# Kernel tuning notes

Measured on AMD Instinct MI355X. Metric: run time of the kernel, lower is better.

The kernel has to match this reference:

```python
import math
import jax, jax.numpy as jnp
import numpy as np

EPS = 1e-08
W_BLK = 256  # covers max window w = exp(log 255) + 1 = 256


def _l2norm(x):
    n = jnp.linalg.norm(x, axis=-1, keepdims=True)
    return x / jnp.maximum(n, EPS)


def setup_inputs() -> dict:
    key = jax.random.key(0)
    ks = jax.random.split(key, 7)
    B, T, Dm, H = 2, 4096, 1024, 16
    scale = 1.0 / math.sqrt(Dm)
    return {
        "query": jax.random.normal(ks[0], (B, T, Dm), jnp.float32),
        "key": jax.random.normal(ks[1], (B, T, Dm), jnp.float32),
        "value": jax.random.normal(ks[2], (B, T, Dm), jnp.float32),
        "Wq": jax.random.normal(ks[3], (Dm, Dm), jnp.float32) * scale,
        "Wk": jax.random.normal(ks[4], (Dm, Dm), jnp.float32) * scale,
        "Wv": jax.random.normal(ks[5], (Dm, Dm), jnp.float32) * scale,
        "Wo": jax.random.normal(ks[6], (Dm, Dm), jnp.float32) * scale,
        "s_v": jnp.linspace(0.0, math.log(255.0), H).astype(jnp.float32),
        "s_r": jnp.zeros((H,), jnp.float32),
    }


def _screening_forward(query, key, value, Wq, Wk, Wv, Wo, s_v, s_r):
    B, T, Dm = query.shape
    H = s_v.shape[0]
    D = Dm // H

    def proj(x, Wm):  # nn.Linear (no bias): x @ W^T, then split heads -> [B,H,T,D]
        return (x @ Wm.T).reshape(B, T, H, D).transpose(0, 2, 1, 3)

    q = _l2norm(proj(query, Wq))
    k = _l2norm(proj(key, Wk))
    v = _l2norm(proj(value, Wv))

    w = jnp.exp(s_v) + 1.0  # [H] window widths, <= 256
    r = jnp.exp(s_r) + 1.0  # [H] screening sharpness

    Wb = W_BLK
    nb = T // Wb
    qb = q.reshape(B, H, nb, Wb, D)
    kb = k.reshape(B, H, nb, Wb, D)
    vb = v.reshape(B, H, nb, Wb, D)
    # each query block attends to its own block + previous block (window <= Wb)
    kprev = jnp.pad(kb, ((0, 0), (0, 0), (1, 0), (0, 0), (0, 0)))[:, :, :nb]
    vprev = jnp.pad(vb, ((0, 0), (0, 0), (1, 0), (0, 0), (0, 0)))[:, :, :nb]
    kc = jnp.concatenate([kprev, kb], axis=3)  # [B,H,nb,2W,D]
    vc = jnp.concatenate([vprev, vb], axis=3)

    sim = jnp.einsum('bhnid,bhnjd->bhnij', qb, kc)  # [B,H,nb,W,2W]

    ii = jnp.arange(Wb)[:, None]
    jj = jnp.arange(2 * Wb)[None, :]
    rel = (jj - (Wb + ii)).astype(jnp.float32)  # [W,2W] relative offset j-i
    wb_ = w[:, None, None]  # [H,1,1]
    cos_m = 0.5 * (jnp.cos(jnp.pi * rel[None] / wb_) + 1.0)  # [H,W,2W]
    in_w = (rel[None] > -wb_) & (rel[None] <= 0.0)  # causal window
    softmask = cos_m * in_w.astype(sim.dtype)  # [H,W,2W]
    # block 0 has no previous block: first Wb key slots invalid there
    blk_valid = ((jnp.arange(nb)[:, None] > 0) | (jnp.arange(2 * Wb)[None, :] >= Wb))

    alpha = jax.nn.relu(1.0 - r[None, :, None, None, None] * (1.0 - sim)) ** 2
    alpha = alpha * softmask[None, :, None] * blk_valid.astype(sim.dtype)[None, None, :, None, :]

    out = jnp.einsum('bhnij,bhnjd->bhnid', alpha, vc).reshape(B, H, T, D)
    # TanhNorm: smoothly bound vector magnitude (tanh of the L2 norm)
    n = jnp.linalg.norm(out, axis=-1, keepdims=True)
    out = out * jnp.tanh(n) / (n + EPS)
    out = out.transpose(0, 2, 1, 3).reshape(B, T, Dm)
    return out @ Wo.T


def reference(query, key, value, Wq, Wk, Wv, Wo, s_v, s_r):
    return _screening_forward(query, key, value, Wq, Wk, Wv, Wo, s_v, s_r)
```

## Files before the change

### kernel.cpp

```cpp
#include <hip/hip_runtime.h>
#include <math.h>

#ifndef M_PI
#define M_PI 3.14159265358979323846
#endif

typedef short bf16x8 __attribute__((ext_vector_type(8)));
typedef _Float16 f16x8 __attribute__((ext_vector_type(8)));
typedef float f32x4 __attribute__((ext_vector_type(4)));

#define LDS_STRIDE 40

union FragU { uint4 u; bf16x8 f; };
union F16U { uint4 u; f16x8 f; _Float16 h[8]; };

__device__ __forceinline__ unsigned rn_hi(float x) {
    unsigned u = __float_as_uint(x);
    unsigned r = u + 0x7FFFu + ((u >> 16) & 1u);
    return r & 0xFFFF0000u;
}

__global__ void mask_tab_kernel(const float* __restrict__ s_v, float* __restrict__ tab) {
    int h = blockIdx.x;
    int idx = threadIdx.x;
    float w = expf(s_v[h]) + 1.0f;
    float rel = (float)(idx - 255);
    float val = 0.0f;
    if (rel > -w) {
        val = 0.5f * (cosf((float)M_PI * rel / w) + 1.0f);
    }
    tab[h * 256 + idx] = val;
}

__device__ __forceinline__ void split8_f16(_Float16* ph, _Float16* pl, int off,
                                           f32x4 x0, f32x4 x1) {
    float xs[8] = {x0[0], x0[1], x0[2], x0[3], x1[0], x1[1], x1[2], x1[3]};
    F16U H, L;
#pragma unroll
    for (int e = 0; e < 8; e++) {
        _Float16 h = (_Float16)xs[e];
        _Float16 l = (_Float16)(xs[e] - (float)h);
        H.h[e] = h;
        L.h[e] = l;
    }
    *(uint4*)(ph + off) = H.u;
    *(uint4*)(pl + off) = L.u;
}

__device__ __forceinline__ void load_ab(const float* aptr, const float* bptr, int kt,
                                        f32x4* ab, f32x4* bb) {
#pragma unroll
    for (int m = 0; m < 4; m++) {
        ab[m] = *(const f32x4*)(aptr + kt + m * 4);
        bb[m] = *(const f32x4*)(bptr + kt + m * 4);
    }
}

__device__ __forceinline__ void stage_ab(_Float16* AhP, _Float16* AlP,
                                         _Float16* BhP, _Float16* BlP, int soff,
                                         const f32x4* ab, const f32x4* bb) {
    split8_f16(AhP, AlP, soff,     ab[0], ab[1]);
    split8_f16(AhP, AlP, soff + 8, ab[2], ab[3]);
    split8_f16(BhP, BlP, soff,     bb[0], bb[1]);
    split8_f16(BhP, BlP, soff + 8, bb[2], bb[3]);
}

__device__ __forceinline__ void compute_tile(const _Float16* AhP, const _Float16* AlP,
                                             const _Float16* BhP, const _Float16* BlP,
                                             int aoff, int boff, f32x4 acc[4][4]) {
#define MFMA_TILE(AF, BF)                                                            \
    do {                                                                             \
        _Pragma("unroll") for (int fr = 0; fr < 4; fr++)                             \
            _Pragma("unroll") for (int fc = 0; fc < 4; fc++)                         \
                acc[fr][fc] = __builtin_amdgcn_mfma_f32_16x16x32_f16(                \
                    AF[fr], BF[fc], acc[fr][fc], 0, 0, 0);                           \
    } while (0)
    f16x8 ah[4], bh[4], t1[4], t2[4];
#pragma unroll
    for (int f = 0; f < 4; f++) {
        ah[f] = *(const f16x8*)&AhP[aoff + f * 16 * LDS_STRIDE];
        bh[f] = *(const f16x8*)&BhP[boff + f * 16 * LDS_STRIDE];
    }
    MFMA_TILE(ah, bh);
#pragma unroll
    for (int f = 0; f < 4; f++)
        t1[f] = *(const f16x8*)&BlP[boff + f * 16 * LDS_STRIDE];
    MFMA_TILE(ah, t1);
#pragma unroll
    for (int f = 0; f < 4; f++)
        t2[f] = *(const f16x8*)&AlP[aoff + f * 16 * LDS_STRIDE];
    MFMA_TILE(t2, bh);
#undef MFMA_TILE
}

template <int PERM>
__global__ __launch_bounds__(256, 2) void gemm_f16x3(const float* __restrict__ A,
                                                     const float* __restrict__ Bm,
                                                     float* __restrict__ C,
                                                     int M, int N, int K) {
    __shared__ _Float16 Ah[2][128 * LDS_STRIDE];
    __shared__ _Float16 Al[2][128 * LDS_STRIDE];
    __shared__ _Float16 Bh[2][128 * LDS_STRIDE];
    __shared__ _Float16 Bl[2][128 * LDS_STRIDE];

    const int tid = threadIdx.x;
    const int bid = blockIdx.x;
    const int swz = (bid & 7) * ((int)gridDim.x >> 3) + (bid >> 3);
    const int brow = (swz >> 3) * 128;
    const int bcol = (swz & 7) * 128;

    const int lane = tid & 63;
    const int wv = tid >> 6;
    const int wr = wv >> 1;
    const int wc = wv & 1;

    const int srow = tid >> 1;
    const int skb = (tid & 1) * 16;
    const float* aptr = A + (size_t)(brow + srow) * K + skb;
    const float* bptr = Bm + (size_t)(bcol + srow) * K + skb;
    const int soff = srow * LDS_STRIDE + skb;

    const int l15 = lane & 15;
    const int k8 = (lane >> 4) * 8;
    const int aoff = (wr * 64 + l15) * LDS_STRIDE + k8;
    const int boff = (wc * 64 + l15) * LDS_STRIDE + k8;

    f32x4 acc[4][4];
#pragma unroll
    for (int a = 0; a < 4; a++)
#pragma unroll
        for (int b = 0; b < 4; b++) acc[a][b] = (f32x4)(0.0f);

    const int nt = K >> 5;
    f32x4 a0[4], b0[4], a1[4], b1[4];
    load_ab(aptr, bptr, 0, a0, b0);
    load_ab(aptr, bptr, 32, a1, b1);
    stage_ab(Ah[0], Al[0], Bh[0], Bl[0], soff, a0, b0);
    __syncthreads();

#pragma unroll 1
    for (int t = 0; t < nt; t += 2) {
        if (t + 2 < nt) load_ab(aptr, bptr, (t + 2) * 32, a0, b0);
        stage_ab(Ah[1], Al[1], Bh[1], Bl[1], soff, a1, b1);
        compute_tile(Ah[0], Al[0], Bh[0], Bl[0], aoff, boff, acc);
        __syncthreads();
        if (t + 3 < nt) load_ab(aptr, bptr, (t + 3) * 32, a1, b1);
        if (t + 2 < nt) stage_ab(Ah[0], Al[0], Bh[0], Bl[0], soff, a0, b0);
        compute_tile(Ah[1], Al[1], Bh[1], Bl[1], aoff, boff, acc);
        __syncthreads();
    }

    if (PERM == 1) {
#pragma unroll
        for (int fr = 0; fr < 4; fr++) {
#pragma unroll
            for (int r = 0; r < 4; r++) {
                float p = 0.0f;
#pragma unroll
                for (int fc = 0; fc < 4; fc++)
                    p = fmaf(acc[fr][fc][r], acc[fr][fc][r], p);
                p += __shfl_xor(p, 1);
                p += __shfl_xor(p, 2);
                p += __shfl_xor(p, 4);
                p += __shfl_xor(p, 8);
                float inv = 1.0f / fmaxf(sqrtf(p), 1e-8f);
#pragma unroll
                for (int fc = 0; fc < 4; fc++) acc[fr][fc][r] *= inv;
            }
        }
    }

    const int rsub = (lane >> 4) * 4;
#pragma unroll
    for (int fr = 0; fr < 4; fr++) {
#pragma unroll
        for (int fc = 0; fc < 4; fc++) {
            f32x4 v = acc[fr][fc];
            const int i0 = brow + wr * 64 + fr * 16 + rsub;
            const int j = bcol + wc * 64 + fc * 16 + l15;
            if (PERM == 0) {
#pragma unroll
                for (int r = 0; r < 4; r++) C[(size_t)(i0 + r) * N + j] = v[r];
            } else {
                const int h = j >> 6;
                const int d = j & 63;
#pragma unroll
                for (int r = 0; r < 4; r++) {
                    const int i = i0 + r;
                    const int b = i >> 12;
                    const int t = i & 4095;
                    C[(((size_t)(b * 16 + h) * 4096 + t) * 64 + d)] = v[r];
                }
            }
        }
    }
}

__global__ __launch_bounds__(256, 3) void attn_kernel(
        const float* __restrict__ q, const float* __restrict__ k,
        const float* __restrict__ v, const float* __restrict__ s_v,
        const float* __restrict__ s_r, const float* __restrict__ mask_tab,
        float* __restrict__ out) {
    __shared__ unsigned short Kh[32 * 72];
    __shared__ unsigned short Kl[32 * 72];
    __shared__ unsigned short Vh[64 * 40];
    __shared__ unsigned short Vl[64 * 40];
    __shared__ unsigned int   aB[4][32 * 33];
    __shared__ float          msk[256];

    const int bx = blockIdx.x;
    const int h   = bx & 15;
    const int n   = (bx >> 4) & 15;
    const int sub = (bx >> 8) & 1;
    const int b   = bx >> 9;
    const int bh = b * 16 + h;
    const int tid = threadIdx.x;
    const int lane = tid & 63;
    const int wid = tid >> 6;
    const int l15 = lane & 15;
    const int g = lane >> 4;

    msk[tid] = mask_tab[h * 256 + tid];
    const float w = expf(s_v[h]) + 1.0f;
    const float rh = expf(s_r[h]) + 1.0f;

    const int row0 = n * 256 + sub * 128;
    const float* qbase = q + (size_t)bh * 4096 * 64;
    const float* kbase = k + (size_t)bh * 4096 * 64;
    const float* vbase = v + (size_t)bh * 4096 * 64;

    bf16x8 qh[2][2], ql[2][2];
#pragma unroll
    for (int f = 0; f < 2; f++) {
#pragma unroll
        for (int ks = 0; ks < 2; ks++) {
            const float* src = qbase + (size_t)(row0 + wid * 32 + f * 16 + l15) * 64
                               + ks * 32 + g * 8;
            f32x4 x0 = *(const f32x4*)src;
            f32x4 x1 = *(const f32x4*)(src + 4);
            float xs[8] = {x0[0], x0[1], x0[2], x0[3], x1[0], x1[1], x1[2], x1[3]};
            unsigned hb[8], lb[8];
#pragma unroll
            for (int e = 0; e < 8; e++) {
                hb[e] = rn_hi(xs[e]);
                lb[e] = rn_hi(xs[e] - __uint_as_float(hb[e]));
            }
            FragU th, tl;
            th.u = make_uint4((hb[0] >> 16) | hb[1], (hb[2] >> 16) | hb[3],
                              (hb[4] >> 16) | hb[5], (hb[6] >> 16) | hb[7]);
            tl.u = make_uint4((lb[0] >> 16) | lb[1], (lb[2] >> 16) | lb[3],
                              (lb[4] >> 16) | lb[5], (lb[6] >> 16) | lb[7]);
            qh[f][ks] = th.f;
            ql[f][ks] = tl.f;
        }
    }

    int jlo = (int)floorf(256.0f + (float)(sub * 128) - w) + 1;
    if (jlo < 0) jlo = 0;
    if (n == 0 && jlo < 256) jlo = 256;
    jlo &= ~31;
    const int jhi = 256 + sub * 128 + 127;

    const int iw0 = sub * 128 + wid * 32;

    f32x4 acc[2][4];
#pragma unroll
    for (int a = 0; a < 2; a++)
#pragma unroll
        for (int d = 0; d < 4; d++) acc[a][d] = (f32x4)(0.0f);

    const int kj = tid >> 3;
    const int kd = (tid & 7) * 8;
    const int vj = tid & 31;
    const int vd = (tid >> 5) * 8;

    f32x4 kr0, kr1, vr0, vr1;
    {
        const float* ks = kbase + (size_t)((n - 1) * 256 + jlo + kj) * 64 + kd;
        const float* vs = vbase + (size_t)((n - 1) * 256 + jlo + vj) * 64 + vd;
        kr0 = *(const f32x4*)ks;  kr1 = *(const f32x4*)(ks + 4);
        vr0 = *(const f32x4*)vs;  vr1 = *(const f32x4*)(vs + 4);
    }

    for (int jt = jlo; jt <= jhi; jt += 32) {
        __syncthreads();
        {
            float xs[8] = {kr0[0], kr0[1], kr0[2], kr0[3], kr1[0], kr1[1], kr1[2], kr1[3]};
            unsigned hb[8], lb[8];
#pragma unroll
            for (int e = 0; e < 8; e++) {
                hb[e] = rn_hi(xs[e]);
                lb[e] = rn_hi(xs[e] - __uint_as_float(hb[e]));
            }
            *(uint4*)&Kh[kj * 72 + kd] =
                make_uint4((hb[0] >> 16) | hb[1], (hb[2] >> 16) | hb[3],
                           (hb[4] >> 16) | hb[5], (hb[6] >> 16) | hb[7]);
            *(uint4*)&Kl[kj * 72 + kd] =
                make_uint4((lb[0] >> 16) | lb[1], (lb[2] >> 16) | lb[3],
                           (lb[4] >> 16) | lb[5], (lb[6] >> 16) | lb[7]);
        }
        {
            float xs[8] = {vr0[0], vr0[1], vr0[2], vr0[3], vr1[0], vr1[1], vr1[2], vr1[3]};
#pragma unroll
            for (int e = 0; e < 8; e++) {
                unsigned hbv = rn_hi(xs[e]);
                unsigned lbv = rn_hi(xs[e] - __uint_as_float(hbv));
                Vh[(vd + e) * 40 + vj] = (unsigned short)(hbv >> 16);
                Vl[(vd + e) * 40 + vj] = (unsigned short)(lbv >> 16);
            }
        }
        if (jt + 32 <= jhi) {
            const float* ks = kbase + (size_t)((n - 1) * 256 + jt + 32 + kj) * 64 + kd;
            const float* vs = vbase + (size_t)((n - 1) * 256 + jt + 32 + vj) * 64 + vd;
            kr0 = *(const f32x4*)ks;  kr1 = *(const f32x4*)(ks + 4);
            vr0 = *(const f32x4*)vs;  vr1 = *(const f32x4*)(vs + 4);
        }
        __syncthreads();

        const bool live = ((float)(jt + 31) > 256.0f + (float)iw0 - w) &&
                          (jt <= 256 + iw0 + 31);
        if (live) {
            f32x4 sim[2][2];
#pragma unroll
            for (int jf = 0; jf < 2; jf++)
#pragma unroll
                for (int f = 0; f < 2; f++) sim[jf][f] = (f32x4)(0.0f);

#pragma unroll
            for (int jf = 0; jf < 2; jf++) {
#pragma unroll
                for (int ks = 0; ks < 2; ks++) {
                    bf16x8 kah = *(const bf16x8*)&Kh[(jf * 16 + l15) * 72 + ks * 32 + g * 8];
                    bf16x8 kal = *(const bf16x8*)&Kl[(jf * 16 + l15) * 72 + ks * 32 + g * 8];
#pragma unroll
                    for (int f = 0; f < 2; f++) {
                        sim[jf][f] = __builtin_amdgcn_mfma_f32_16x16x32_bf16(
                            kah, qh[f][ks], sim[jf][f], 0, 0, 0);
                        sim[jf][f] = __builtin_amdgcn_mfma_f32_16x16x32_bf16(
                            kah, ql[f][ks], sim[jf][f], 0, 0, 0);
                        sim[jf][f] = __builtin_amdgcn_mfma_f32_16x16x32_bf16(
                            kal, qh[f][ks], sim[jf][f], 0, 0, 0);
                    }
                }
            }

#pragma unroll
            for (int jf = 0; jf < 2; jf++) {
#pragma unroll
                for (int f = 0; f < 2; f++) {
#pragma unroll
                    for (int r = 0; r < 4; r++) {
                        const int jloc = jf * 16 + g * 4 + r;
                        const int iloc = f * 16 + l15;
                        const int relv = (jt + jloc) - 256 - (sub * 128 + wid * 32 + iloc);
                        float m = (relv >= -255 && relv <= 0) ? msk[relv + 255] : 0.0f;
                        float t1 = 1.0f - rh * (1.0f - sim[jf][f][r]);
                        t1 = fmaxf(t1, 0.0f);
                        float alpha = t1 * t1 * m;
                        unsigned ahb = rn_hi(alpha);
                        unsigned alb = rn_hi(alpha - __uint_as_float(ahb));
                        aB[wid][jloc * 33 + iloc] = ahb | (alb >> 16);
                    }
                }
            }

#pragma unroll
            for (int f = 0; f < 2; f++) {
                unsigned a8[8];
#pragma unroll
                for (int e = 0; e < 8; e++)
                    a8[e] = aB[wid][(g * 8 + e) * 33 + f * 16 + l15];
                FragU th, tl;
                th.u = make_uint4((a8[0] >> 16) | (a8[1] & 0xFFFF0000u),
                                  (a8[2] >> 16) | (a8[3] & 0xFFFF0000u),
                                  (a8[4] >> 16) | (a8[5] & 0xFFFF0000u),
                                  (a8[6] >> 16) | (a8[7] & 0xFFFF0000u));
                tl.u = make_uint4((a8[0] << 16 >> 16) | (a8[1] << 16),
                                  (a8[2] << 16 >> 16) | (a8[3] << 16),
                                  (a8[4] << 16 >> 16) | (a8[5] << 16),
                                  (a8[6] << 16 >> 16) | (a8[7] << 16));
                bf16x8 aah = th.f, aal = tl.f;
#pragma unroll
                for (int df = 0; df < 4; df++) {
                    bf16x8 vbh = *(const bf16x8*)&Vh[(df * 16 + l15) * 40 + g * 8];
                    bf16x8 vbl = *(const bf16x8*)&Vl[(df * 16 + l15) * 40 + g * 8];
                    acc[f][df] = __builtin_amdgcn_mfma_f32_16x16x32_bf16(
                        aah, vbh, acc[f][df], 0, 0, 0);
                    acc[f][df] = __builtin_amdgcn_mfma_f32_16x16x32_bf16(
                        aah, vbl, acc[f][df], 0, 0, 0);
                    acc[f][df] = __builtin_amdgcn_mfma_f32_16x16x32_bf16(
                        aal, vbh, acc[f][df], 0, 0, 0);
                }
            }
        }
    }

#pragma unroll
    for (int f = 0; f < 2; f++) {
#pragma unroll
        for (int r = 0; r < 4; r++) {
            float p = 0.0f;
#pragma unroll
            for (int df = 0; df < 4; df++) p = fmaf(acc[f][df][r], acc[f][df][r], p);
            p += __shfl_xor(p, 1);
            p += __shfl_xor(p, 2);
            p += __shfl_xor(p, 4);
            p += __shfl_xor(p, 8);
            float nn = sqrtf(p);
            float sc = tanhf(nn) / (nn + 1e-8f);
            const int trow = row0 + wid * 32 + f * 16 + g * 4 + r;
            float* dst = out + ((size_t)(b * 4096 + trow)) * 1024 + h * 64;
#pragma unroll
            for (int df = 0; df < 4; df++)
                dst[df * 16 + l15] = acc[f][df][r] * sc;
        }
    }
}

extern "C" void kernel_launch(void* const* d_in, const int* in_sizes, int n_in,
                              void* d_out, int out_size, void* d_ws, size_t ws_size,
                              hipStream_t stream) {
    const float* query = (const float*)d_in[0];
    const float* key   = (const float*)d_in[1];
    const float* value = (const float*)d_in[2];
    const float* Wq    = (const float*)d_in[3];
    const float* Wk    = (const float*)d_in[4];
    const float* Wv    = (const float*)d_in[5];
    const float* Wo    = (const float*)d_in[6];
    const float* s_v   = (const float*)d_in[7];
    const float* s_r   = (const float*)d_in[8];
    float* out = (float*)d_out;

    const size_t PROJ = (size_t)2 * 16 * 4096 * 64;
    float* qw = (float*)d_ws;
    float* kw = qw + PROJ;
    float* vw = kw + PROJ;
    float* ao = vw + PROJ;
    float* mask = ao + PROJ;

    mask_tab_kernel<<<dim3(16), dim3(256), 0, stream>>>(s_v, mask);

    gemm_f16x3<1><<<dim3(512), dim3(256), 0, stream>>>(query, Wq, qw, 8192, 1024, 1024);
    gemm_f16x3<1><<<dim3(512), dim3(256), 0, stream>>>(key,   Wk, kw, 8192, 1024, 1024);
    gemm_f16x3<1><<<dim3(512), dim3(256), 0, stream>>>(value, Wv, vw, 8192, 1024, 1024);

    attn_kernel<<<dim3(1024), dim3(256), 0, stream>>>(qw, kw, vw, s_v, s_r, mask, ao);

    gemm_f16x3<0><<<dim3(512), dim3(256), 0, stream>>>(ao, Wo, out, 8192, 1024, 1024);
}
```

Baseline: 338.3 us.

## Pre-split fp16 hi/lo tiles and stream them into LDS via direct global loads

Adds a pre-pass that converts the activations and weights into swizzled fp16 hi/lo tile blobs. A new GEMM kernel then loads these tiles straight into LDS with global_load_lds and runs the 3-term f16 MFMA, so the fp32-to-f16 split no longer sits inside the GEMM inner loop. The Q/K/V projections are merged into a single launch. This costs extra workspace and extra passes that write and read the split copies. The original path is kept as a fallback when the workspace is too small.

```diff
diff --git a/kernel.cpp b/kernel.cpp
--- a/kernel.cpp
+++ b/kernel.cpp
@@ -13,6 +13,9 @@
 
 union FragU { uint4 u; bf16x8 f; };
 union F16U { uint4 u; f16x8 f; _Float16 h[8]; };
+
+typedef const __attribute__((address_space(1))) void GVoid;
+typedef __attribute__((address_space(3))) void LVoid;
 
 __device__ __forceinline__ unsigned rn_hi(float x) {
     unsigned u = __float_as_uint(x);
@@ -30,6 +33,173 @@
         val = 0.5f * (cosf((float)M_PI * rel / w) + 1.0f);
     }
     tab[h * 256 + idx] = val;
+}
+
+__global__ __launch_bounds__(256) void split_tiles(
+        const float* __restrict__ in0, const float* __restrict__ in1,
+        const float* __restrict__ in2, const float* __restrict__ in3,
+        char* __restrict__ out0, unsigned long long ostride) {
+    const float* in = (blockIdx.y == 0) ? in0 : (blockIdx.y == 1) ? in1
+                    : (blockIdx.y == 2) ? in2 : in3;
+    char* outp = out0 + (size_t)blockIdx.y * ostride;
+    const int tile = blockIdx.x;
+    const int kt = tile & 31;
+    const int rb = tile >> 5;
+    const int tid = threadIdx.x;
+    const int row = tid >> 1;
+    const int kc = (tid & 1) * 16;
+
+    const float* src = in + ((size_t)(rb * 128 + row)) * 1024 + kt * 32 + kc;
+    f32x4 x0 = *(const f32x4*)src;
+    f32x4 x1 = *(const f32x4*)(src + 4);
+    f32x4 x2 = *(const f32x4*)(src + 8);
+    f32x4 x3 = *(const f32x4*)(src + 12);
+    float xs[16] = {x0[0], x0[1], x0[2], x0[3], x1[0], x1[1], x1[2], x1[3],
+                    x2[0], x2[1], x2[2], x2[3], x3[0], x3[1], x3[2], x3[3]};
+    F16U h0, h1, l0, l1;
+#pragma unroll
+    for (int e = 0; e < 8; e++) {
+        _Float16 h = (_Float16)xs[e];
+        h0.h[e] = h;
+        l0.h[e] = (_Float16)(xs[e] - (float)h);
+        _Float16 h2 = (_Float16)xs[8 + e];
+        h1.h[e] = h2;
+        l1.h[e] = (_Float16)(xs[8 + e] - (float)h2);
+    }
+    char* tb = outp + (size_t)tile * 16384 + row * 128;
+    const int swz = (row & 7) << 4;
+    *(uint4*)(tb + ((kc * 2) ^ swz))       = h0.u;
+    *(uint4*)(tb + ((kc * 2 + 16) ^ swz))  = h1.u;
+    *(uint4*)(tb + ((64 + kc * 2) ^ swz))  = l0.u;
+    *(uint4*)(tb + ((64 + kc * 2 + 16) ^ swz)) = l1.u;
+}
+
+template <int PERM>
+__global__ __launch_bounds__(256, 3) void gemm_t3(
+        const char* __restrict__ Abase, unsigned long long Astride,
+        const char* __restrict__ Bbase, unsigned long long Bstride,
+        float* __restrict__ C0, float* __restrict__ C1, float* __restrict__ C2) {
+    __shared__ __align__(16) char lds[32768];
+
+    const int tid = threadIdx.x;
+    const int bid = blockIdx.x;
+    const int o = bid >> 9;
+    const int b2 = bid & 511;
+    const char* At = Abase + (size_t)o * Astride;
+    const char* Bt = Bbase + (size_t)o * Bstride;
+    float* C = (o == 0) ? C0 : (o == 1) ? C1 : C2;
+
+    const int swzb = (b2 & 7) * 64 + (b2 >> 3);
+    const int brow = (swzb >> 3) * 128;
+    const int bcol = (swzb & 7) * 128;
+
+    const int lane = tid & 63;
+    const int wid = tid >> 6;
+    const int wr = wid >> 1;
+    const int wc = wid & 1;
+    const int l15 = lane & 15;
+    const int g = lane >> 4;
+
+    const char* Atile0 = At + ((size_t)(brow >> 7) * 32) * 16384;
+    const char* Btile0 = Bt + ((size_t)(bcol >> 7) * 32) * 16384;
+    const int sbase = wid * 4096;
+
+    const int swzr = (l15 & 7) << 4;
+    const int aoff = (wr * 64 + l15) * 128 + ((g * 16) ^ swzr);
+    const int boff = 16384 + (wc * 64 + l15) * 128 + ((g * 16) ^ swzr);
+
+    f32x4 acc[4][4];
+#pragma unroll
+    for (int a = 0; a < 4; a++)
+#pragma unroll
+        for (int b = 0; b < 4; b++) acc[a][b] = (f32x4)(0.0f);
+
+#define MFMA_T3(AF, BF)                                                              \
+    do {                                                                             \
+        _Pragma("unroll") for (int fr = 0; fr < 4; fr++)                             \
+            _Pragma("unroll") for (int fc = 0; fc < 4; fc++)                         \
+                acc[fr][fc] = __builtin_amdgcn_mfma_f32_16x16x32_f16(                \
+                    AF[fr], BF[fc], acc[fr][fc], 0, 0, 0);                           \
+    } while (0)
+
+#pragma unroll 1
+    for (int kt = 0; kt < 32; kt++) {
+        __syncthreads();
+        const char* As = Atile0 + kt * 16384 + sbase;
+        const char* Bs = Btile0 + kt * 16384 + sbase;
+#pragma unroll
+        for (int is = 0; is < 4; is++) {
+            __builtin_amdgcn_global_load_lds(
+                (GVoid*)(As + is * 1024 + lane * 16),
+                (LVoid*)(lds + sbase + is * 1024), 16, 0, 0);
+            __builtin_amdgcn_global_load_lds(
+                (GVoid*)(Bs + is * 1024 + lane * 16),
+                (LVoid*)(lds + 16384 + sbase + is * 1024), 16, 0, 0);
+        }
+        __syncthreads();
+
+        f16x8 ah[4], bh[4], t[4];
+#pragma unroll
+        for (int f = 0; f < 4; f++) {
+            ah[f] = *(const f16x8*)(lds + aoff + f * 2048);
+            bh[f] = *(const f16x8*)(lds + boff + f * 2048);
+        }
+        MFMA_T3(ah, bh);
+#pragma unroll
+        for (int f = 0; f < 4; f++)
+            t[f] = *(const f16x8*)(lds + (boff ^ 64) + f * 2048);
+        MFMA_T3(ah, t);
+#pragma unroll
+        for (int f = 0; f < 4; f++)
+            t[f] = *(const f16x8*)(lds + (aoff ^ 64) + f * 2048);
+        MFMA_T3(t, bh);
+    }
+#undef MFMA_T3
+
+    if (PERM == 1) {
+#pragma unroll
+        for (int fr = 0; fr < 4; fr++) {
+#pragma unroll
+            for (int r = 0; r < 4; r++) {
+                float p = 0.0f;
+#pragma unroll
+                for (int fc = 0; fc < 4; fc++)
+                    p = fmaf(acc[fr][fc][r], acc[fr][fc][r], p);
+                p += __shfl_xor(p, 1);
+                p += __shfl_xor(p, 2);
+                p += __shfl_xor(p, 4);
+                p += __shfl_xor(p, 8);
+                float inv = 1.0f / fmaxf(sqrtf(p), 1e-8f);
+#pragma unroll
+                for (int fc = 0; fc < 4; fc++) acc[fr][fc][r] *= inv;
+            }
+        }
+    }
+
+    const int rsub = (lane >> 4) * 4;
+#pragma unroll
+    for (int fr = 0; fr < 4; fr++) {
+#pragma unroll
+        for (int fc = 0; fc < 4; fc++) {
+            f32x4 v = acc[fr][fc];
+            const int i0 = brow + wr * 64 + fr * 16 + rsub;
+            const int j = bcol + wc * 64 + fc * 16 + l15;
+            if (PERM == 0) {
+#pragma unroll
+                for (int r = 0; r < 4; r++) C[(size_t)(i0 + r) * 1024 + j] = v[r];
+            } else {
+                const int h = j >> 6;
+                const int d = j & 63;
+#pragma unroll
+                for (int r = 0; r < 4; r++) {
+                    const int i = i0 + r;
+                    const int b = i >> 12;
+                    const int t2 = i & 4095;
+                    C[(((size_t)(b * 16 + h) * 4096 + t2) * 64 + d)] = v[r];
+                }
+            }
+        }
+    }
 }
 
 __device__ __forceinline__ void split8_f16(_Float16* ph, _Float16* pl, int off,
@@ -188,8 +358,8 @@
                 for (int r = 0; r < 4; r++) {
                     const int i = i0 + r;
                     const int b = i >> 12;
-                    const int t = i & 4095;
-                    C[(((size_t)(b * 16 + h) * 4096 + t) * 64 + d)] = v[r];
+                    const int t2 = i & 4095;
+                    C[(((size_t)(b * 16 + h) * 4096 + t2) * 64 + d)] = v[r];
                 }
             }
         }
@@ -431,20 +601,38 @@
     const float* s_r   = (const float*)d_in[8];
     float* out = (float*)d_out;
 
-    const size_t PROJ = (size_t)2 * 16 * 4096 * 64;
-    float* qw = (float*)d_ws;
-    float* kw = qw + PROJ;
-    float* vw = kw + PROJ;
-    float* ao = vw + PROJ;
-    float* mask = ao + PROJ;
+    const size_t MB = 1ull << 20;
+    char* base = (char*)d_ws;
+    float* qw   = (float*)(base + 0 * MB);
+    float* kw   = (float*)(base + 32 * MB);
+    float* vw   = (float*)(base + 64 * MB);
+    float* ao   = (float*)(base + 96 * MB);
+    float* mask = (float*)(base + 128 * MB);
+    char* xsp  = base + 128 * MB + 65536;
+    char* wsp  = xsp + 96 * MB;
+    char* aosp = wsp + 16 * MB;
+    const size_t NEED = 128 * MB + 65536 + 96 * MB + 16 * MB + 32 * MB;
 
     mask_tab_kernel<<<dim3(16), dim3(256), 0, stream>>>(s_v, mask);
 
-    gemm_f16x3<1><<<dim3(512), dim3(256), 0, stream>>>(query, Wq, qw, 8192, 1024, 1024);
-    gemm_f16x3<1><<<dim3(512), dim3(256), 0, stream>>>(key,   Wk, kw, 8192, 1024, 1024);
-    gemm_f16x3<1><<<dim3(512), dim3(256), 0, stream>>>(value, Wv, vw, 8192, 1024, 1024);
-
-    attn_kernel<<<dim3(1024), dim3(256), 0, stream>>>(qw, kw, vw, s_v, s_r, mask, ao);
-
-    gemm_f16x3<0><<<dim3(512), dim3(256), 0, stream>>>(ao, Wo, out, 8192, 1024, 1024);
-}
+    if (ws_size >= NEED) {
+        split_tiles<<<dim3(2048, 3), dim3(256), 0, stream>>>(
+            query, key, value, nullptr, xsp, 32 * MB);
+        split_tiles<<<dim3(256, 4), dim3(256), 0, stream>>>(
+            Wq, Wk, Wv, Wo, wsp, 4 * MB);
+        gemm_t3<1><<<dim3(1536), dim3(256), 0, stream>>>(
+            xsp, 32 * MB, wsp, 4 * MB, qw, kw, vw);
+        attn_kernel<<<dim3(1024), dim3(256), 0, stream>>>(
+            qw, kw, vw, s_v, s_r, mask, ao);
+        split_tiles<<<dim3(2048, 1), dim3(256), 0, stream>>>(
+            ao, nullptr, nullptr, nullptr, aosp, 0);
+        gemm_t3<0><<<dim3(512), dim3(256), 0, stream>>>(
+            aosp, 0, wsp + 12 * MB, 0, out, out, out);
+    } else {
+        gemm_f16x3<1><<<dim3(512), dim3(256), 0, stream>>>(query, Wq, qw, 8192, 1024, 1024);
+        gemm_f16x3<1><<<dim3(512), dim3(256), 0, stream>>>(key,   Wk, kw, 8192, 1024, 1024);
+        gemm_f16x3<1><<<dim3(512), dim3(256), 0, stream>>>(value, Wv, vw, 8192, 1024, 1024);
+        attn_kernel<<<dim3(1024), dim3(256), 0, stream>>>(qw, kw, vw, s_v, s_r, mask, ao);
+        gemm_f16x3<0><<<dim3(512), dim3(256), 0, stream>>>(ao, Wo, out, 8192, 1024, 1024);
+    }
+}
```

New measurement: 338.6 us. Within noise of the previous version (+0.1%).

## Pre-split weights to fp16 hi/lo tiles and batch QKV GEMMs

Applied to the files above, without the earlier changes.

The weights are now pre-split into swizzled fp16 hi/lo tiles by a separate kernel, and B tiles are streamed straight into LDS with global_load_lds. The A-side split is done in registers and overlapped with the MFMA loop. The three Q/K/V projections become one launch with a 128x256 block tile and XCD-aware block mapping, so each block reuses its A tile across twice as many columns. This removes the per-block conversion of weight tiles and cuts the number of launches. The costs are extra split kernels, a larger 80KB LDS footprint that limits occupancy, and workspace aliasing where ao overlaps w3sp and wosp overlaps qw.

```diff
diff --git a/kernel.cpp b/kernel.cpp
--- a/kernel.cpp
+++ b/kernel.cpp
@@ -9,10 +9,11 @@
 typedef _Float16 f16x8 __attribute__((ext_vector_type(8)));
 typedef float f32x4 __attribute__((ext_vector_type(4)));
 
-#define LDS_STRIDE 40
-
 union FragU { uint4 u; bf16x8 f; };
 union F16U { uint4 u; f16x8 f; _Float16 h[8]; };
+
+typedef const __attribute__((address_space(1))) void GVoid;
+typedef __attribute__((address_space(3))) void LVoid;
 
 __device__ __forceinline__ unsigned rn_hi(float x) {
     unsigned u = __float_as_uint(x);
@@ -32,122 +33,166 @@
     tab[h * 256 + idx] = val;
 }
 
-__device__ __forceinline__ void split8_f16(_Float16* ph, _Float16* pl, int off,
-                                           f32x4 x0, f32x4 x1) {
-    float xs[8] = {x0[0], x0[1], x0[2], x0[3], x1[0], x1[1], x1[2], x1[3]};
-    F16U H, L;
+__global__ __launch_bounds__(256) void split_tiles(
+        const float* __restrict__ in0, const float* __restrict__ in1,
+        const float* __restrict__ in2, char* __restrict__ out0,
+        unsigned long long ostride) {
+    const float* in = (blockIdx.y == 0) ? in0 : (blockIdx.y == 1) ? in1 : in2;
+    char* outp = out0 + (size_t)blockIdx.y * ostride;
+    const int tile = blockIdx.x;
+    const int kt = tile & 31;
+    const int rb = tile >> 5;
+    const int tid = threadIdx.x;
+    const int row = tid >> 1;
+    const int kc = (tid & 1) * 16;
+
+    const float* src = in + ((size_t)(rb * 128 + row)) * 1024 + kt * 32 + kc;
+    f32x4 x0 = *(const f32x4*)src;
+    f32x4 x1 = *(const f32x4*)(src + 4);
+    f32x4 x2 = *(const f32x4*)(src + 8);
+    f32x4 x3 = *(const f32x4*)(src + 12);
+    float xs[16] = {x0[0], x0[1], x0[2], x0[3], x1[0], x1[1], x1[2], x1[3],
+                    x2[0], x2[1], x2[2], x2[3], x3[0], x3[1], x3[2], x3[3]};
+    F16U h0, h1, l0, l1;
 #pragma unroll
     for (int e = 0; e < 8; e++) {
         _Float16 h = (_Float16)xs[e];
-        _Float16 l = (_Float16)(xs[e] - (float)h);
-        H.h[e] = h;
-        L.h[e] = l;
-    }
-    *(uint4*)(ph + off) = H.u;
-    *(uint4*)(pl + off) = L.u;
-}
-
-__device__ __forceinline__ void load_ab(const float* aptr, const float* bptr, int kt,
-                                        f32x4* ab, f32x4* bb) {
-#pragma unroll
-    for (int m = 0; m < 4; m++) {
-        ab[m] = *(const f32x4*)(aptr + kt + m * 4);
-        bb[m] = *(const f32x4*)(bptr + kt + m * 4);
-    }
-}
-
-__device__ __forceinline__ void stage_ab(_Float16* AhP, _Float16* AlP,
-                                         _Float16* BhP, _Float16* BlP, int soff,
-                                         const f32x4* ab, const f32x4* bb) {
-    split8_f16(AhP, AlP, soff,     ab[0], ab[1]);
-    split8_f16(AhP, AlP, soff + 8, ab[2], ab[3]);
-    split8_f16(BhP, BlP, soff,     bb[0], bb[1]);
-    split8_f16(BhP, BlP, soff + 8, bb[2], bb[3]);
-}
-
-__device__ __forceinline__ void compute_tile(const _Float16* AhP, const _Float16* AlP,
-                                             const _Float16* BhP, const _Float16* BlP,
-                                             int aoff, int boff, f32x4 acc[4][4]) {
-#define MFMA_TILE(AF, BF)                                                            \
-    do {                                                                             \
-        _Pragma("unroll") for (int fr = 0; fr < 4; fr++)                             \
-            _Pragma("unroll") for (int fc = 0; fc < 4; fc++)                         \
-                acc[fr][fc] = __builtin_amdgcn_mfma_f32_16x16x32_f16(                \
-                    AF[fr], BF[fc], acc[fr][fc], 0, 0, 0);                           \
-    } while (0)
-    f16x8 ah[4], bh[4], t1[4], t2[4];
-#pragma unroll
-    for (int f = 0; f < 4; f++) {
-        ah[f] = *(const f16x8*)&AhP[aoff + f * 16 * LDS_STRIDE];
-        bh[f] = *(const f16x8*)&BhP[boff + f * 16 * LDS_STRIDE];
-    }
-    MFMA_TILE(ah, bh);
-#pragma unroll
-    for (int f = 0; f < 4; f++)
-        t1[f] = *(const f16x8*)&BlP[boff + f * 16 * LDS_STRIDE];
-    MFMA_TILE(ah, t1);
-#pragma unroll
-    for (int f = 0; f < 4; f++)
-        t2[f] = *(const f16x8*)&AlP[aoff + f * 16 * LDS_STRIDE];
-    MFMA_TILE(t2, bh);
-#undef MFMA_TILE
+        h0.h[e] = h;
+        l0.h[e] = (_Float16)(xs[e] - (float)h);
+        _Float16 h2 = (_Float16)xs[8 + e];
+        h1.h[e] = h2;
+        l1.h[e] = (_Float16)(xs[8 + e] - (float)h2);
+    }
+    char* tb = outp + (size_t)tile * 16384 + row * 128;
+    const int swz = (row & 7) << 4;
+    *(uint4*)(tb + ((kc * 2) ^ swz))           = h0.u;
+    *(uint4*)(tb + ((kc * 2 + 16) ^ swz))      = h1.u;
+    *(uint4*)(tb + ((64 + kc * 2) ^ swz))      = l0.u;
+    *(uint4*)(tb + ((64 + kc * 2 + 16) ^ swz)) = l1.u;
+}
+
+__device__ __forceinline__ void cvt_split16(const f32x4* a, F16U& h0, F16U& h1,
+                                            F16U& l0, F16U& l1) {
+    float xs[16] = {a[0][0], a[0][1], a[0][2], a[0][3],
+                    a[1][0], a[1][1], a[1][2], a[1][3],
+                    a[2][0], a[2][1], a[2][2], a[2][3],
+                    a[3][0], a[3][1], a[3][2], a[3][3]};
+#pragma unroll
+    for (int e = 0; e < 8; e++) {
+        _Float16 h = (_Float16)xs[e];
+        h0.h[e] = h;
+        l0.h[e] = (_Float16)(xs[e] - (float)h);
+        _Float16 h2 = (_Float16)xs[8 + e];
+        h1.h[e] = h2;
+        l1.h[e] = (_Float16)(xs[8 + e] - (float)h2);
+    }
 }
 
 template <int PERM>
-__global__ __launch_bounds__(256, 2) void gemm_f16x3(const float* __restrict__ A,
-                                                     const float* __restrict__ Bm,
-                                                     float* __restrict__ C,
-                                                     int M, int N, int K) {
-    __shared__ _Float16 Ah[2][128 * LDS_STRIDE];
-    __shared__ _Float16 Al[2][128 * LDS_STRIDE];
-    __shared__ _Float16 Bh[2][128 * LDS_STRIDE];
-    __shared__ _Float16 Bl[2][128 * LDS_STRIDE];
+__global__ __launch_bounds__(256, 2) void gemm_ws(
+        const float* __restrict__ A0, const float* __restrict__ A1,
+        const float* __restrict__ A2,
+        const char* __restrict__ Bsp, unsigned long long Bstride,
+        float* __restrict__ C0, float* __restrict__ C1, float* __restrict__ C2) {
+    __shared__ __align__(16) char Abuf[16384];
+    __shared__ __align__(16) char Bbuf[65536];
 
     const int tid = threadIdx.x;
     const int bid = blockIdx.x;
-    const int swz = (bid & 7) * ((int)gridDim.x >> 3) + (bid >> 3);
-    const int brow = (swz >> 3) * 128;
-    const int bcol = (swz & 7) * 128;
+    const int o = bid >> 8;
+    const int x = bid & 255;
+    const int xcd = x & 7;
+    const int idx = x >> 3;
+    const int rp = xcd * 8 + (idx >> 2);
+    const int cp = idx & 3;
+    const int brow = rp * 128;
+    const int bcol = cp * 256;
+
+    const float* A = (o == 0) ? A0 : (o == 1) ? A1 : A2;
+    float* C = (o == 0) ? C0 : (o == 1) ? C1 : C2;
+    const char* Bt = Bsp + (size_t)o * Bstride;
 
     const int lane = tid & 63;
-    const int wv = tid >> 6;
-    const int wr = wv >> 1;
-    const int wc = wv & 1;
+    const int wid = tid >> 6;
+    const int wr = wid >> 1;
+    const int wc = wid & 1;
+    const int l15 = lane & 15;
+    const int g = lane >> 4;
 
     const int srow = tid >> 1;
-    const int skb = (tid & 1) * 16;
-    const float* aptr = A + (size_t)(brow + srow) * K + skb;
-    const float* bptr = Bm + (size_t)(bcol + srow) * K + skb;
-    const int soff = srow * LDS_STRIDE + skb;
-
-    const int l15 = lane & 15;
-    const int k8 = (lane >> 4) * 8;
-    const int aoff = (wr * 64 + l15) * LDS_STRIDE + k8;
-    const int boff = (wc * 64 + l15) * LDS_STRIDE + k8;
-
-    f32x4 acc[4][4];
+    const int skc2 = (tid & 1) * 32;
+    const float* aptr = A + (size_t)(brow + srow) * 1024 + (tid & 1) * 16;
+    const int aswz = (srow & 7) << 4;
+    char* awr = Abuf + srow * 128;
+
+    const char* bsrc = Bt + ((size_t)(cp * 2 + (wid >> 1)) * 32) * 16384
+                       + (wid & 1) * 8192;
+
+    const int rswz = (l15 & 7) << 4;
+
+    f32x4 acc[4][8];
 #pragma unroll
     for (int a = 0; a < 4; a++)
 #pragma unroll
-        for (int b = 0; b < 4; b++) acc[a][b] = (f32x4)(0.0f);
-
-    const int nt = K >> 5;
-    f32x4 a0[4], b0[4], a1[4], b1[4];
-    load_ab(aptr, bptr, 0, a0, b0);
-    load_ab(aptr, bptr, 32, a1, b1);
-    stage_ab(Ah[0], Al[0], Bh[0], Bl[0], soff, a0, b0);
-    __syncthreads();
+        for (int b = 0; b < 8; b++) acc[a][b] = (f32x4)(0.0f);
+
+    f32x4 areg[4];
+#pragma unroll
+    for (int m = 0; m < 4; m++) areg[m] = *(const f32x4*)(aptr + m * 4);
+    F16U Sh0, Sh1, Sl0, Sl1;
+    cvt_split16(areg, Sh0, Sh1, Sl0, Sl1);
+#pragma unroll
+    for (int i = 0; i < 8; i++)
+        __builtin_amdgcn_global_load_lds(
+            (GVoid*)(bsrc + i * 1024 + lane * 16),
+            (LVoid*)(Bbuf + wid * 8192 + i * 1024), 16, 0, 0);
 
 #pragma unroll 1
-    for (int t = 0; t < nt; t += 2) {
-        if (t + 2 < nt) load_ab(aptr, bptr, (t + 2) * 32, a0, b0);
-        stage_ab(Ah[1], Al[1], Bh[1], Bl[1], soff, a1, b1);
-        compute_tile(Ah[0], Al[0], Bh[0], Bl[0], aoff, boff, acc);
+    for (int kt = 0; kt < 32; kt++) {
         __syncthreads();
-        if (t + 3 < nt) load_ab(aptr, bptr, (t + 3) * 32, a1, b1);
-        if (t + 2 < nt) stage_ab(Ah[0], Al[0], Bh[0], Bl[0], soff, a0, b0);
-        compute_tile(Ah[1], Al[1], Bh[1], Bl[1], aoff, boff, acc);
+        *(uint4*)(awr + ((skc2) ^ aswz))      = Sh0.u;
+        *(uint4*)(awr + ((skc2 + 16) ^ aswz)) = Sh1.u;
+        *(uint4*)(awr + ((skc2 + 64) ^ aswz)) = Sl0.u;
+        *(uint4*)(awr + ((skc2 + 80) ^ aswz)) = Sl1.u;
         __syncthreads();
+
+        if (kt + 1 < 32) {
+            const char* bs = bsrc + (size_t)(kt + 1) * 16384;
+            const int nxt = ((kt + 1) & 1) * 32768;
+#pragma unroll
+            for (int i = 0; i < 8; i++)
+                __builtin_amdgcn_global_load_lds(
+                    (GVoid*)(bs + i * 1024 + lane * 16),
+                    (LVoid*)(Bbuf + nxt + wid * 8192 + i * 1024), 16, 0, 0);
+#pragma unroll
+            for (int m = 0; m < 4; m++)
+                areg[m] = *(const f32x4*)(aptr + (kt + 1) * 32 + m * 4);
+        }
+
+        const char* bb = Bbuf + (kt & 1) * 32768 + wc * 16384;
+        f16x8 ah[4], al[4];
+#pragma unroll
+        for (int fr = 0; fr < 4; fr++) {
+            const int ro = (wr * 64 + fr * 16 + l15) * 128;
+            ah[fr] = *(const f16x8*)(Abuf + ro + ((g * 16) ^ rswz));
+            al[fr] = *(const f16x8*)(Abuf + ro + ((g * 16) ^ rswz ^ 64));
+        }
+#pragma unroll
+        for (int fc = 0; fc < 8; fc++) {
+            const int ro = (fc * 16 + l15) * 128;
+            f16x8 bh = *(const f16x8*)(bb + ro + ((g * 16) ^ rswz));
+            f16x8 bl = *(const f16x8*)(bb + ro + ((g * 16) ^ rswz ^ 64));
+#pragma unroll
+            for (int fr = 0; fr < 4; fr++) {
+                acc[fr][fc] = __builtin_amdgcn_mfma_f32_16x16x32_f16(
+                    ah[fr], bh, acc[fr][fc], 0, 0, 0);
+                acc[fr][fc] = __builtin_amdgcn_mfma_f32_16x16x32_f16(
+                    ah[fr], bl, acc[fr][fc], 0, 0, 0);
+                acc[fr][fc] = __builtin_amdgcn_mfma_f32_16x16x32_f16(
+                    al[fr], bh, acc[fr][fc], 0, 0, 0);
+            }
+        }
+        if (kt + 1 < 32) cvt_split16(areg, Sh0, Sh1, Sl0, Sl1);
     }
 
     if (PERM == 1) {
@@ -155,41 +200,48 @@
         for (int fr = 0; fr < 4; fr++) {
 #pragma unroll
             for (int r = 0; r < 4; r++) {
-                float p = 0.0f;
-#pragma unroll
-                for (int fc = 0; fc < 4; fc++)
-                    p = fmaf(acc[fr][fc][r], acc[fr][fc][r], p);
-                p += __shfl_xor(p, 1);
-                p += __shfl_xor(p, 2);
-                p += __shfl_xor(p, 4);
-                p += __shfl_xor(p, 8);
-                float inv = 1.0f / fmaxf(sqrtf(p), 1e-8f);
-#pragma unroll
-                for (int fc = 0; fc < 4; fc++) acc[fr][fc][r] *= inv;
-            }
-        }
-    }
-
-    const int rsub = (lane >> 4) * 4;
+                float p0 = 0.0f, p1 = 0.0f;
+#pragma unroll
+                for (int fc = 0; fc < 4; fc++) {
+                    p0 = fmaf(acc[fr][fc][r], acc[fr][fc][r], p0);
+                    p1 = fmaf(acc[fr][fc + 4][r], acc[fr][fc + 4][r], p1);
+                }
+                p0 += __shfl_xor(p0, 1);  p1 += __shfl_xor(p1, 1);
+                p0 += __shfl_xor(p0, 2);  p1 += __shfl_xor(p1, 2);
+                p0 += __shfl_xor(p0, 4);  p1 += __shfl_xor(p1, 4);
+                p0 += __shfl_xor(p0, 8);  p1 += __shfl_xor(p1, 8);
+                float i0 = 1.0f / fmaxf(sqrtf(p0), 1e-8f);
+                float i1 = 1.0f / fmaxf(sqrtf(p1), 1e-8f);
+#pragma unroll
+                for (int fc = 0; fc < 4; fc++) {
+                    acc[fr][fc][r] *= i0;
+                    acc[fr][fc + 4][r] *= i1;
+                }
+            }
+        }
+    }
+
+    const int rsub = g * 4;
 #pragma unroll
     for (int fr = 0; fr < 4; fr++) {
 #pragma unroll
-        for (int fc = 0; fc < 4; fc++) {
+        for (int fc = 0; fc < 8; fc++) {
             f32x4 v = acc[fr][fc];
             const int i0 = brow + wr * 64 + fr * 16 + rsub;
-            const int j = bcol + wc * 64 + fc * 16 + l15;
+            const int j0 = bcol + wc * 128 + fc * 16;
             if (PERM == 0) {
 #pragma unroll
-                for (int r = 0; r < 4; r++) C[(size_t)(i0 + r) * N + j] = v[r];
+                for (int r = 0; r < 4; r++)
+                    C[(size_t)(i0 + r) * 1024 + j0 + l15] = v[r];
             } else {
-                const int h = j >> 6;
-                const int d = j & 63;
+                const int h = j0 >> 6;
+                const int d = (j0 & 63) + l15;
 #pragma unroll
                 for (int r = 0; r < 4; r++) {
                     const int i = i0 + r;
                     const int b = i >> 12;
-                    const int t = i & 4095;
-                    C[(((size_t)(b * 16 + h) * 4096 + t) * 64 + d)] = v[r];
+                    const int t2 = i & 4095;
+                    C[(((size_t)(b * 16 + h) * 4096 + t2) * 64 + d)] = v[r];
                 }
             }
         }
@@ -431,20 +483,28 @@
     const float* s_r   = (const float*)d_in[8];
     float* out = (float*)d_out;
 
-    const size_t PROJ = (size_t)2 * 16 * 4096 * 64;
-    float* qw = (float*)d_ws;
-    float* kw = qw + PROJ;
-    float* vw = kw + PROJ;
-    float* ao = vw + PROJ;
-    float* mask = ao + PROJ;
+    const size_t MB = 1ull << 20;
+    char* base = (char*)d_ws;
+    float* qw   = (float*)(base);
+    float* kw   = (float*)(base + 32 * MB);
+    float* vw   = (float*)(base + 64 * MB);
+    float* ao   = (float*)(base + 96 * MB);
+    char*  w3sp = base + 96 * MB;
+    char*  wosp = base;
+    float* mask = (float*)(base + 128 * MB);
 
     mask_tab_kernel<<<dim3(16), dim3(256), 0, stream>>>(s_v, mask);
 
-    gemm_f16x3<1><<<dim3(512), dim3(256), 0, stream>>>(query, Wq, qw, 8192, 1024, 1024);
-    gemm_f16x3<1><<<dim3(512), dim3(256), 0, stream>>>(key,   Wk, kw, 8192, 1024, 1024);
-    gemm_f16x3<1><<<dim3(512), dim3(256), 0, stream>>>(value, Wv, vw, 8192, 1024, 1024);
-
-    attn_kernel<<<dim3(1024), dim3(256), 0, stream>>>(qw, kw, vw, s_v, s_r, mask, ao);
-
-    gemm_f16x3<0><<<dim3(512), dim3(256), 0, stream>>>(ao, Wo, out, 8192, 1024, 1024);
-}
+    split_tiles<<<dim3(256, 3), dim3(256), 0, stream>>>(Wq, Wk, Wv, w3sp, 4 * MB);
+
+    gemm_ws<1><<<dim3(768), dim3(256), 0, stream>>>(
+        query, key, value, w3sp, 4 * MB, qw, kw, vw);
+
+    attn_kernel<<<dim3(1024), dim3(256), 0, stream>>>(
+        qw, kw, vw, s_v, s_r, mask, ao);
+
+    split_tiles<<<dim3(256, 1), dim3(256), 0, stream>>>(Wo, Wo, Wo, wosp, 0);
+
+    gemm_ws<0><<<dim3(256), dim3(256), 0, stream>>>(
+        ao, ao, ao, wosp, 0, out, out, out);
+}
```

After: 328.9 us. 2.8% less time.
